# Kernel tuning notes

Hardware: AMD Instinct MI355X
Metric: run time of the kernel (lower is better)

The kernel has to match this reference:

```python
import jax, jax.numpy as jnp
import numpy as np

B, N, D = 8, 1024, 768
H, Z = 12, 64          # num_heads, head_dim (D = H*Z)
HID = 3072             # int(D * mlp_ratio)


def setup_inputs() -> dict:
    key = jax.random.key(0)
    k1, k2, k3, k4 = jax.random.split(key, 4)
    s = 0.02
    x = jax.random.normal(k1, (B, N, D), dtype=jnp.float32)
    Wq = jax.random.normal(k2, (D, D), dtype=jnp.float32) * s
    Wk = jax.random.normal(k3, (D, D), dtype=jnp.float32) * s
    betas = jnp.full((H,), Z ** -0.5, dtype=jnp.float32)
    W_mlp = jax.random.normal(k4, (HID, D), dtype=jnp.float32) * s
    return {"x": x, "Wq": Wq, "Wk": Wk, "betas": betas, "W_mlp": W_mlp}


def reference(x, Wq, Wk, betas, W_mlp):
    # --- KQ-aligned attention ---
    # torch Linear: y = x @ W.T ; weight shape [out=D, in=D]
    Q = jnp.einsum('bnd,ed->bne', x, Wq).reshape(B, N, H, Z).transpose(0, 2, 1, 3)  # bhqz
    K = jnp.einsum('bnd,ed->bne', x, Wk).reshape(B, N, H, Z).transpose(0, 2, 1, 3)  # bhkz
    Wq_r = Wq.reshape(H, Z, D)
    Wk_r = Wk.reshape(H, Z, D)
    F1 = jnp.einsum('hzd,bhkz->bkhd', Wq_r, K)
    F2 = jnp.einsum('hzd,bhqz->bqhd', Wk_r, Q)
    scores = jnp.einsum('bhqz,bhkz,h->bhqk', Q, K, betas)
    attn = jax.nn.softmax(scores, axis=-1)
    T1 = jnp.einsum('bkhd,bhqk->bqd', F1, attn)
    T2 = jnp.einsum('bqhd,bhqk->bkd', F2, attn)
    # --- symmetric-weight Hopfield MLP (bias=False) ---
    hid = jax.nn.relu(jnp.einsum('bnd,hd->bnh', x, W_mlp))
    mlp = jnp.einsum('bnh,hd->bnd', hid, W_mlp)
    return T1 + T2 + mlp
```

## Files before the change

kernel.cpp:

```cpp
#include <hip/hip_runtime.h>
#include <hip/hip_bf16.h>

#define Bq 8
#define Nq 1024
#define Dq 768
#define Hq 12
#define Zq 64
#define HIDq 3072
#define BN (Bq*Nq)
#define QKP 1536

typedef unsigned short u16;
typedef short s16x8 __attribute__((ext_vector_type(8)));
typedef float f32x4 __attribute__((ext_vector_type(4)));
typedef unsigned short u16x4 __attribute__((ext_vector_type(4)));

#define MFMA16 __builtin_amdgcn_mfma_f32_16x16x32_bf16
#define GLOAD16(g, l) __builtin_amdgcn_global_load_lds( \
    (const __attribute__((address_space(1))) void*)(const void*)(g), \
    (__attribute__((address_space(3))) void*)(l), 16, 0, 0)

__device__ __forceinline__ u16 f2bf(float f) {
  unsigned u = __float_as_uint(f);
  return (u16)((u + 0x7FFFu + ((u >> 16) & 1u)) >> 16);
}

__device__ __forceinline__ void xcd_swizzle(int gx, int gy, int& bx, int& by) {
  int l = blockIdx.y * gx + blockIdx.x;
  int c = l & 7, j = l >> 3;
  by = c * (gy >> 3) + j / gx;
  bx = j % gx;
}

__global__ __launch_bounds__(256) void cvt_bf16(const float* __restrict__ in,
                                                u16* __restrict__ out, int n) {
  int i = (blockIdx.x * 256 + threadIdx.x) * 4;
  if (i >= n) return;
  float4 v = *(const float4*)&in[i];
  u16x4 o; o[0] = f2bf(v.x); o[1] = f2bf(v.y); o[2] = f2bf(v.z); o[3] = f2bf(v.w);
  *(u16x4*)&out[i] = o;
}

__global__ __launch_bounds__(256) void cvt_tr(const float* __restrict__ in,
                                              u16* __restrict__ out, u16* __restrict__ outT,
                                              int C, int out_p, int outT_p) {
  __shared__ u16 T[64][72];
  const int t = threadIdx.x;
  const int r0 = blockIdx.y * 64, c0 = blockIdx.x * 64;
  const int r = t >> 3, c8 = (t & 7) * 8;
#pragma unroll
  for (int p = 0; p < 2; p++) {
    const float* ip = &in[(size_t)(r0 + r + p * 32) * C + c0 + c8];
    float4 v0 = *(const float4*)ip, v1 = *(const float4*)(ip + 4);
    u16 tmp[8] = {f2bf(v0.x), f2bf(v0.y), f2bf(v0.z), f2bf(v0.w),
                  f2bf(v1.x), f2bf(v1.y), f2bf(v1.z), f2bf(v1.w)};
    *(uint4*)&out[(size_t)(r0 + r + p * 32) * out_p + c0 + c8] = *(uint4*)tmp;
    *(uint4*)&T[r + p * 32][c8] = *(uint4*)tmp;
  }
  __syncthreads();
#pragma unroll
  for (int p = 0; p < 2; p++) {
    int oc = r + p * 32;
    u16 tmp[8];
#pragma unroll
    for (int j = 0; j < 8; j++) tmp[j] = T[c8 + j][oc];
    *(uint4*)&outT[(size_t)(c0 + oc) * outT_p + r0 + c8] = *(uint4*)tmp;
  }
}

__global__ __launch_bounds__(256) void transpose_bf16(
    const u16* __restrict__ in, u16* __restrict__ out,
    int in_pitch, int out_pitch, int inner_n,
    long in_bs_o, long in_bs_i, long out_bs_o, long out_bs_i) {
  __shared__ u16 T[64][72];
  const int t = threadIdx.x;
  const int bz = blockIdx.z;
  const long iboff = (long)(bz / inner_n) * in_bs_o + (long)(bz % inner_n) * in_bs_i;
  const long oboff = (long)(bz / inner_n) * out_bs_o + (long)(bz % inner_n) * out_bs_i;
  const u16* ip = in + iboff + (long)(blockIdx.y * 64) * in_pitch + blockIdx.x * 64;
  u16* op = out + oboff + (long)(blockIdx.x * 64) * out_pitch + blockIdx.y * 64;
  const int r = t >> 3, c8 = (t & 7) * 8;
#pragma unroll
  for (int p = 0; p < 2; p++)
    *(uint4*)&T[r + p * 32][c8] = *(const uint4*)(ip + (size_t)(r + p * 32) * in_pitch + c8);
  __syncthreads();
#pragma unroll
  for (int p = 0; p < 2; p++) {
    int oc = r + p * 32;
    u16 tmp[8];
#pragma unroll
    for (int j = 0; j < 8; j++) tmp[j] = T[c8 + j][oc];
    *(uint4*)(op + (size_t)oc * out_pitch + c8) = *(uint4*)tmp;
  }
}

template<bool RELU>
__global__ __launch_bounds__(256) void gemm_bf16(
    const u16* __restrict__ A, const u16* __restrict__ B, u16* __restrict__ C,
    int M, int N, int K) {
  __shared__ u16 As[2][128 * 32];
  __shared__ u16 Bs[2][128 * 32];
  int bx, by;
  xcd_swizzle(gridDim.x, gridDim.y, bx, by);
  const int t = threadIdx.x, l = t & 63, w = t >> 6;
  const int lq = l & 15, quad = l >> 4;
  const int bm = by * 128, bn = bx * 128;
  const int wm = (w & 1) * 64, wn = (w >> 1) * 64;
  f32x4 acc[4][4];
#pragma unroll
  for (int i = 0; i < 4; i++)
#pragma unroll
    for (int j = 0; j < 4; j++) acc[i][j] = (f32x4){0.f, 0.f, 0.f, 0.f};

  auto stage = [&](int k0, int bufi) {
#pragma unroll
    for (int p = 0; p < 2; p++) {
      int idx = p * 256 + t;
      GLOAD16(A + (size_t)(bm + (idx >> 2)) * K + k0 + (idx & 3) * 8, &As[bufi][idx * 8]);
      GLOAD16(B + (size_t)(bn + (idx >> 2)) * K + k0 + (idx & 3) * 8, &Bs[bufi][idx * 8]);
    }
  };
  stage(0, 0);
  const int nIter = K >> 5;
  for (int it = 0; it < nIter; it++) {
    __syncthreads();
    if (it + 1 < nIter) stage((it + 1) * 32, (it + 1) & 1);
    const int bi = it & 1;
    s16x8 af[4], bf[4];
#pragma unroll
    for (int mt = 0; mt < 4; mt++)
      af[mt] = *(const s16x8*)&As[bi][(wm + mt * 16 + lq) * 32 + quad * 8];
#pragma unroll
    for (int nt = 0; nt < 4; nt++)
      bf[nt] = *(const s16x8*)&Bs[bi][(wn + nt * 16 + lq) * 32 + quad * 8];
#pragma unroll
    for (int mt = 0; mt < 4; mt++)
#pragma unroll
      for (int nt = 0; nt < 4; nt++)
        acc[mt][nt] = MFMA16(af[mt], bf[nt], acc[mt][nt], 0, 0, 0);
  }
#pragma unroll
  for (int mt = 0; mt < 4; mt++)
#pragma unroll
    for (int nt = 0; nt < 4; nt++) {
      int row = bm + wm + mt * 16 + quad * 4;
      int col = bn + wn + nt * 16 + lq;
#pragma unroll
      for (int r = 0; r < 4; r++) {
        float v = acc[mt][nt][r];
        if (RELU) v = fmaxf(v, 0.f);
        C[(size_t)(row + r) * N + col] = f2bf(v);
      }
    }
}

__global__ __launch_bounds__(256) void gemm_out2(
    const u16* __restrict__ AV12, const u16* __restrict__ hid,
    const u16* __restrict__ WqkT, const u16* __restrict__ WmT,
    float* __restrict__ out) {
  __shared__ u16 As[2][128 * 64];
  __shared__ u16 Bs[2][64 * 64];
  int bx, by;
  xcd_swizzle(gridDim.x, gridDim.y, bx, by);
  const int t = threadIdx.x, l = t & 63, w = t >> 6;
  const int lq = l & 15, quad = l >> 4;
  const int bm = by * 128, bn = bx * 64;
  const int wm = w * 32;
  f32x4 acc[2][4];
#pragma unroll
  for (int i = 0; i < 2; i++)
#pragma unroll
    for (int j = 0; j < 4; j++) acc[i][j] = (f32x4){0.f, 0.f, 0.f, 0.f};

  auto stage = [&](int tl, int bufi) {
    const u16* A; const u16* B; int pitch, k0;
    if (tl < 24) { A = AV12; B = WqkT; pitch = QKP;  k0 = tl * 64; }
    else         { A = hid;  B = WmT;  pitch = HIDq; k0 = (tl - 24) * 64; }
#pragma unroll
    for (int p = 0; p < 4; p++) {
      int idx = p * 256 + t, ks = idx >> 9, rem = idx & 511;
      GLOAD16(A + (size_t)(bm + (rem >> 2)) * pitch + k0 + ks * 32 + (rem & 3) * 8,
              &As[bufi][idx * 8]);
    }
#pragma unroll
    for (int p = 0; p < 2; p++) {
      int idx = p * 256 + t, ks = idx >> 8, rem = idx & 255;
      GLOAD16(B + (size_t)(bn + (rem >> 2)) * pitch + k0 + ks * 32 + (rem & 3) * 8,
              &Bs[bufi][idx * 8]);
    }
  };
  stage(0, 0);
  for (int tl = 0; tl < 72; tl++) {
    __syncthreads();
    if (tl + 1 < 72) stage(tl + 1, (tl + 1) & 1);
    const int bi = tl & 1;
#pragma unroll
    for (int ks = 0; ks < 2; ks++) {
      s16x8 af[2], bf[4];
#pragma unroll
      for (int mt = 0; mt < 2; mt++)
        af[mt] = *(const s16x8*)&As[bi][ks * 4096 + (wm + mt * 16 + lq) * 32 + quad * 8];
#pragma unroll
      for (int nt = 0; nt < 4; nt++)
        bf[nt] = *(const s16x8*)&Bs[bi][ks * 2048 + (nt * 16 + lq) * 32 + quad * 8];
#pragma unroll
      for (int mt = 0; mt < 2; mt++)
#pragma unroll
        for (int nt = 0; nt < 4; nt++)
          acc[mt][nt] = MFMA16(af[mt], bf[nt], acc[mt][nt], 0, 0, 0);
    }
  }
#pragma unroll
  for (int mt = 0; mt < 2; mt++)
#pragma unroll
    for (int nt = 0; nt < 4; nt++) {
      int row = bm + wm + mt * 16 + quad * 4;
      int col = bn + nt * 16 + lq;
#pragma unroll
      for (int r = 0; r < 4; r++)
        out[(size_t)(row + r) * Dq + col] = acc[mt][nt][r];
    }
}

__global__ __launch_bounds__(256) void attn_pass1(
    const u16* __restrict__ QKb, const u16* __restrict__ KbT,
    const float* __restrict__ betas, u16* __restrict__ AV12,
    float* __restrict__ lg) {
  __shared__ u16 Qs[2][64][32];
  __shared__ u16 Ks[2][2][64][32];
  __shared__ u16 Kts[2][2][64][32];
  __shared__ u16 Ps[64][72];
  __shared__ float red[4][64];
  __shared__ float li[64];

  const int t = threadIdx.x, l = t & 63, w = t >> 6;
  const int lq = l & 15, quad = l >> 4;
  const int c = blockIdx.x & 7, j = blockIdx.x >> 3;
  const int bh = c * 12 + j / 16, qt = j % 16;
  const int b = bh / Hq, h = bh % Hq;
  const int q0 = qt * 64;
  const float beta = betas[h];
  const u16* Qh = QKb + (size_t)(b * Nq) * QKP + h * 64;
  const u16* Kh = Qh + Dq;
  const u16* KTh = KbT + (size_t)bh * 64 * Nq;
  u16* QsF = &Qs[0][0][0];

#pragma unroll
  for (int p = 0; p < 2; p++) {
    int idx = p * 256 + t;
    GLOAD16(Qh + (size_t)(q0 + ((idx >> 2) & 63)) * QKP + (idx >> 8) * 32 + (idx & 3) * 8,
            QsF + idx * 8);
  }

  auto stageK = [&](int kt, int bufi) {
#pragma unroll
    for (int p = 0; p < 2; p++) {
      int idx = p * 256 + t;
      GLOAD16(Kh + (size_t)(kt * 64 + ((idx >> 2) & 63)) * QKP + (idx >> 8) * 32 + (idx & 3) * 8,
              &Ks[bufi][0][0][0] + idx * 8);
      GLOAD16(KTh + (size_t)((idx >> 2) & 63) * Nq + kt * 64 + (idx >> 8) * 32 + (idx & 3) * 8,
              &Kts[bufi][0][0][0] + idx * 8);
    }
  };
  stageK(0, 0);
  __syncthreads();
  s16x8 bqf[2][4];
#pragma unroll
  for (int zs = 0; zs < 2; zs++)
#pragma unroll
    for (int nt = 0; nt < 4; nt++)
      bqf[zs][nt] = *(const s16x8*)&Qs[zs][nt * 16 + lq][quad * 8];

  float lsum[4] = {0.f, 0.f, 0.f, 0.f};
  f32x4 ao[4];
#pragma unroll
  for (int nt = 0; nt < 4; nt++) ao[nt] = (f32x4){0.f, 0.f, 0.f, 0.f};

  for (int kt = 0; kt < 16; kt++) {
    if (kt) __syncthreads();
    if (kt + 1 < 16) stageK(kt + 1, (kt + 1) & 1);
    const int bi = kt & 1;
    f32x4 sc[4];
#pragma unroll
    for (int nt = 0; nt < 4; nt++) sc[nt] = (f32x4){0.f, 0.f, 0.f, 0.f};
#pragma unroll
    for (int zs = 0; zs < 2; zs++) {
      s16x8 a = *(const s16x8*)&Ks[bi][zs][w * 16 + lq][quad * 8];
#pragma unroll
      for (int nt = 0; nt < 4; nt++)
        sc[nt] = MFMA16(a, bqf[zs][nt], sc[nt], 0, 0, 0);
    }
#pragma unroll
    for (int nt = 0; nt < 4; nt++) {
      u16x4 pk;
#pragma unroll
      for (int r = 0; r < 4; r++) {
        float e = __expf(sc[nt][r] * beta);
        lsum[nt] += e;
        pk[r] = f2bf(e);
      }
      *(u16x4*)&Ps[nt * 16 + lq][w * 16 + quad * 4] = pk;
    }
    __syncthreads();
#pragma unroll
    for (int ks = 0; ks < 2; ks++) {
      s16x8 a = *(const s16x8*)&Ps[w * 16 + lq][ks * 32 + quad * 8];
#pragma unroll
      for (int nt = 0; nt < 4; nt++) {
        s16x8 bk = *(const s16x8*)&Kts[bi][ks][nt * 16 + lq][quad * 8];
        ao[nt] = MFMA16(a, bk, ao[nt], 0, 0, 0);
      }
    }
  }
#pragma unroll
  for (int nt = 0; nt < 4; nt++) {
    float v = lsum[nt];
    v += __shfl_xor(v, 16, 64);
    v += __shfl_xor(v, 32, 64);
    if (l < 16) red[w][nt * 16 + lq] = v;
  }
  __syncthreads();
  if (t < 64) {
    float s = red[0][t] + red[1][t] + red[2][t] + red[3][t];
    lg[(size_t)bh * Nq + q0 + t] = s;
    li[t] = 1.0f / s;
  }
  __syncthreads();
  u16* Oh = AV12 + (size_t)(b * Nq + q0) * QKP + h * 64;
  float lr[4];
#pragma unroll
  for (int r = 0; r < 4; r++) lr[r] = li[w * 16 + quad * 4 + r];
#pragma unroll
  for (int nt = 0; nt < 4; nt++)
#pragma unroll
    for (int r = 0; r < 4; r++)
      Oh[(size_t)(w * 16 + quad * 4 + r) * QKP + nt * 16 + lq] = f2bf(ao[nt][r] * lr[r]);
}

__global__ __launch_bounds__(256) void attn_pass2(
    const u16* __restrict__ QKb, const u16* __restrict__ QbT,
    const float* __restrict__ betas, u16* __restrict__ AV12,
    const float* __restrict__ lg) {
  __shared__ u16 Ks[2][64][32];
  __shared__ u16 Qs[2][2][64][32];
  __shared__ u16 Qts[2][2][64][32];
  __shared__ u16 Pts[64][72];
  __shared__ float li_s[2][64];

  const int t = threadIdx.x, l = t & 63, w = t >> 6;
  const int lq = l & 15, quad = l >> 4;
  const int c = blockIdx.x & 7, j = blockIdx.x >> 3;
  const int bh = c * 12 + j / 16, kt = j % 16;
  const int b = bh / Hq, h = bh % Hq;
  const int k0 = kt * 64;
  const float beta = betas[h];
  const u16* Qh = QKb + (size_t)(b * Nq) * QKP + h * 64;
  const u16* Kh = Qh + Dq;
  const u16* QTh = QbT + (size_t)bh * 64 * Nq;
  u16* KsF = &Ks[0][0][0];

#pragma unroll
  for (int p = 0; p < 2; p++) {
    int idx = p * 256 + t;
    GLOAD16(Kh + (size_t)(k0 + ((idx >> 2) & 63)) * QKP + (idx >> 8) * 32 + (idx & 3) * 8,
            KsF + idx * 8);
  }

  auto stageQ = [&](int qt, int bufi) {
#pragma unroll
    for (int p = 0; p < 2; p++) {
      int idx = p * 256 + t;
      GLOAD16(Qh + (size_t)(qt * 64 + ((idx >> 2) & 63)) * QKP + (idx >> 8) * 32 + (idx & 3) * 8,
              &Qs[bufi][0][0][0] + idx * 8);
      GLOAD16(QTh + (size_t)((idx >> 2) & 63) * Nq + qt * 64 + (idx >> 8) * 32 + (idx & 3) * 8,
              &Qts[bufi][0][0][0] + idx * 8);
    }
    if (t < 64) li_s[bufi][t] = 1.0f / lg[(size_t)bh * Nq + qt * 64 + t];
  };
  stageQ(0, 0);
  __syncthreads();
  s16x8 bkf[2][4];
#pragma unroll
  for (int zs = 0; zs < 2; zs++)
#pragma unroll
    for (int nt = 0; nt < 4; nt++)
      bkf[zs][nt] = *(const s16x8*)&Ks[zs][nt * 16 + lq][quad * 8];

  f32x4 ao[4];
#pragma unroll
  for (int nt = 0; nt < 4; nt++) ao[nt] = (f32x4){0.f, 0.f, 0.f, 0.f};

  for (int qt = 0; qt < 16; qt++) {
    if (qt) __syncthreads();
    if (qt + 1 < 16) stageQ(qt + 1, (qt + 1) & 1);
    const int bi = qt & 1;
    f32x4 sc[4];
#pragma unroll
    for (int nt = 0; nt < 4; nt++) sc[nt] = (f32x4){0.f, 0.f, 0.f, 0.f};
#pragma unroll
    for (int zs = 0; zs < 2; zs++) {
      s16x8 a = *(const s16x8*)&Qs[bi][zs][w * 16 + lq][quad * 8];
#pragma unroll
      for (int nt = 0; nt < 4; nt++)
        sc[nt] = MFMA16(a, bkf[zs][nt], sc[nt], 0, 0, 0);
    }
    float lr[4];
#pragma unroll
    for (int r = 0; r < 4; r++) lr[r] = li_s[bi][w * 16 + quad * 4 + r];
#pragma unroll
    for (int nt = 0; nt < 4; nt++) {
      u16x4 pk;
#pragma unroll
      for (int r = 0; r < 4; r++)
        pk[r] = f2bf(__expf(sc[nt][r] * beta) * lr[r]);
      *(u16x4*)&Pts[nt * 16 + lq][w * 16 + quad * 4] = pk;
    }
    __syncthreads();
#pragma unroll
    for (int qs = 0; qs < 2; qs++) {
      s16x8 a = *(const s16x8*)&Pts[w * 16 + lq][qs * 32 + quad * 8];
#pragma unroll
      for (int nt = 0; nt < 4; nt++) {
        s16x8 bq = *(const s16x8*)&Qts[bi][qs][nt * 16 + lq][quad * 8];
        ao[nt] = MFMA16(a, bq, ao[nt], 0, 0, 0);
      }
    }
  }
  u16* Oh = AV12 + (size_t)(b * Nq + k0) * QKP + Dq + h * 64;
#pragma unroll
  for (int nt = 0; nt < 4; nt++)
#pragma unroll
    for (int r = 0; r < 4; r++)
      Oh[(size_t)(w * 16 + quad * 4 + r) * QKP + nt * 16 + lq] = f2bf(ao[nt][r]);
}

extern "C" void kernel_launch(void* const* d_in, const int* in_sizes, int n_in,
                              void* d_out, int out_size, void* d_ws, size_t ws_size,
                              hipStream_t stream) {
  const float* x     = (const float*)d_in[0];
  const float* Wq    = (const float*)d_in[1];
  const float* Wk    = (const float*)d_in[2];
  const float* betas = (const float*)d_in[3];
  const float* Wm    = (const float*)d_in[4];
  float* out = (float*)d_out;

  u16* xb   = (u16*)d_ws;
  u16* Wqkb = xb + (size_t)BN * Dq;
  u16* Wmb  = Wqkb + (size_t)QKP * Dq;
  u16* WqkT = Wmb + (size_t)HIDq * Dq;
  u16* QKb  = WqkT + (size_t)Dq * QKP;
  u16* QbT  = QKb + (size_t)BN * QKP;
  u16* KbT  = QbT + (size_t)Bq * Hq * Zq * Nq;
  u16* AV12 = KbT + (size_t)Bq * Hq * Zq * Nq;
  float* lg = (float*)(AV12 + (size_t)BN * QKP);
  u16* hidb = QKb;
  u16* WmT  = xb;

  dim3 blk(256);
  cvt_bf16<<<(BN * Dq) / 1024, blk, 0, stream>>>(x, xb, BN * Dq);
  cvt_tr<<<dim3(12, 12), blk, 0, stream>>>(Wq, Wqkb, WqkT, Dq, Dq, QKP);
  cvt_tr<<<dim3(12, 12), blk, 0, stream>>>(Wk, Wqkb + (size_t)Dq * Dq, WqkT + Dq, Dq, Dq, QKP);
  cvt_bf16<<<(HIDq * Dq) / 1024, blk, 0, stream>>>(Wm, Wmb, HIDq * Dq);

  gemm_bf16<false><<<dim3(QKP / 128, BN / 128), blk, 0, stream>>>(
      xb, Wqkb, QKb, BN, QKP, Dq);

  transpose_bf16<<<dim3(1, 16, 96), blk, 0, stream>>>(QKb, QbT, QKP, Nq, Hq,
      (long)Nq * QKP, 64, (long)Hq * 64 * Nq, (long)64 * Nq);
  transpose_bf16<<<dim3(1, 16, 96), blk, 0, stream>>>(QKb + Dq, KbT, QKP, Nq, Hq,
      (long)Nq * QKP, 64, (long)Hq * 64 * Nq, (long)64 * Nq);

  attn_pass1<<<Bq * Hq * 16, blk, 0, stream>>>(QKb, KbT, betas, AV12, lg);
  attn_pass2<<<Bq * Hq * 16, blk, 0, stream>>>(QKb, QbT, betas, AV12, lg);

  gemm_bf16<true><<<dim3(HIDq / 128, BN / 128), blk, 0, stream>>>(
      xb, Wmb, hidb, BN, HIDq, Dq);

  transpose_bf16<<<dim3(12, 48, 1), blk, 0, stream>>>(Wmb, WmT, Dq, HIDq, 1, 0, 0, 0, 0);

  gemm_out2<<<dim3(Dq / 64, BN / 128), blk, 0, stream>>>(AV12, hidb, WqkT, WmT, out);
}
```

Before: 372.4 us.

## Cut attention LDS footprint by single-buffering score operands and aliasing scratch buffers

```diff
diff --git a/kernel.cpp b/kernel.cpp
--- a/kernel.cpp
+++ b/kernel.cpp
@@ -23,6 +23,13 @@
 __device__ __forceinline__ u16 f2bf(float f) {
   unsigned u = __float_as_uint(f);
   return (u16)((u + 0x7FFFu + ((u >> 16) & 1u)) >> 16);
+}
+
+__device__ __forceinline__ unsigned pk2bf(float a, float b) {
+  union { __hip_bfloat162 h; unsigned u; } cv;
+  cv.h.x = __float2bfloat16(a);
+  cv.h.y = __float2bfloat16(b);
+  return cv.u;
 }
 
 __device__ __forceinline__ void xcd_swizzle(int gx, int gy, int& bx, int& by) {
@@ -226,12 +233,9 @@
     const u16* __restrict__ QKb, const u16* __restrict__ KbT,
     const float* __restrict__ betas, u16* __restrict__ AV12,
     float* __restrict__ lg) {
-  __shared__ u16 Qs[2][64][32];
-  __shared__ u16 Ks[2][2][64][32];
+  __shared__ u16 Ps[64][72];
+  __shared__ u16 Ks[2][64][32];
   __shared__ u16 Kts[2][2][64][32];
-  __shared__ u16 Ps[64][72];
-  __shared__ float red[4][64];
-  __shared__ float li[64];
 
   const int t = threadIdx.x, l = t & 63, w = t >> 6;
   const int lq = l & 15, quad = l >> 4;
@@ -243,7 +247,25 @@
   const u16* Qh = QKb + (size_t)(b * Nq) * QKP + h * 64;
   const u16* Kh = Qh + Dq;
   const u16* KTh = KbT + (size_t)bh * 64 * Nq;
-  u16* QsF = &Qs[0][0][0];
+  u16* QsF = &Ps[0][0];
+  u16* KsF = &Ks[0][0][0];
+
+  auto stageK = [&](int kt2) {
+#pragma unroll
+    for (int p = 0; p < 2; p++) {
+      int idx = p * 256 + t;
+      GLOAD16(Kh + (size_t)(kt2 * 64 + ((idx >> 2) & 63)) * QKP + (idx >> 8) * 32 + (idx & 3) * 8,
+              KsF + idx * 8);
+    }
+  };
+  auto stageKt = [&](int kt2, int bufi) {
+#pragma unroll
+    for (int p = 0; p < 2; p++) {
+      int idx = p * 256 + t;
+      GLOAD16(KTh + (size_t)((idx >> 2) & 63) * Nq + kt2 * 64 + (idx >> 8) * 32 + (idx & 3) * 8,
+              &Kts[bufi][0][0][0] + idx * 8);
+    }
+  };
 
 #pragma unroll
   for (int p = 0; p < 2; p++) {
@@ -251,25 +273,16 @@
     GLOAD16(Qh + (size_t)(q0 + ((idx >> 2) & 63)) * QKP + (idx >> 8) * 32 + (idx & 3) * 8,
             QsF + idx * 8);
   }
-
-  auto stageK = [&](int kt, int bufi) {
-#pragma unroll
-    for (int p = 0; p < 2; p++) {
-      int idx = p * 256 + t;
-      GLOAD16(Kh + (size_t)(kt * 64 + ((idx >> 2) & 63)) * QKP + (idx >> 8) * 32 + (idx & 3) * 8,
-              &Ks[bufi][0][0][0] + idx * 8);
-      GLOAD16(KTh + (size_t)((idx >> 2) & 63) * Nq + kt * 64 + (idx >> 8) * 32 + (idx & 3) * 8,
-              &Kts[bufi][0][0][0] + idx * 8);
-    }
-  };
-  stageK(0, 0);
+  stageK(0);
+  stageKt(0, 0);
   __syncthreads();
   s16x8 bqf[2][4];
 #pragma unroll
   for (int zs = 0; zs < 2; zs++)
 #pragma unroll
     for (int nt = 0; nt < 4; nt++)
-      bqf[zs][nt] = *(const s16x8*)&Qs[zs][nt * 16 + lq][quad * 8];
+      bqf[zs][nt] = *(const s16x8*)&QsF[zs * 2048 + (nt * 16 + lq) * 32 + quad * 8];
+  __syncthreads();
 
   float lsum[4] = {0.f, 0.f, 0.f, 0.f};
   f32x4 ao[4];
@@ -278,30 +291,30 @@
 
   for (int kt = 0; kt < 16; kt++) {
     if (kt) __syncthreads();
-    if (kt + 1 < 16) stageK(kt + 1, (kt + 1) & 1);
     const int bi = kt & 1;
     f32x4 sc[4];
 #pragma unroll
     for (int nt = 0; nt < 4; nt++) sc[nt] = (f32x4){0.f, 0.f, 0.f, 0.f};
 #pragma unroll
     for (int zs = 0; zs < 2; zs++) {
-      s16x8 a = *(const s16x8*)&Ks[bi][zs][w * 16 + lq][quad * 8];
+      s16x8 a = *(const s16x8*)&Ks[zs][w * 16 + lq][quad * 8];
 #pragma unroll
       for (int nt = 0; nt < 4; nt++)
         sc[nt] = MFMA16(a, bqf[zs][nt], sc[nt], 0, 0, 0);
     }
 #pragma unroll
     for (int nt = 0; nt < 4; nt++) {
-      u16x4 pk;
-#pragma unroll
-      for (int r = 0; r < 4; r++) {
-        float e = __expf(sc[nt][r] * beta);
-        lsum[nt] += e;
-        pk[r] = f2bf(e);
-      }
-      *(u16x4*)&Ps[nt * 16 + lq][w * 16 + quad * 4] = pk;
+      float e0 = __expf(sc[nt][0] * beta), e1 = __expf(sc[nt][1] * beta);
+      float e2 = __expf(sc[nt][2] * beta), e3 = __expf(sc[nt][3] * beta);
+      lsum[nt] += (e0 + e1) + (e2 + e3);
+      uint2 pk; pk.x = pk2bf(e0, e1); pk.y = pk2bf(e2, e3);
+      *(uint2*)&Ps[nt * 16 + lq][w * 16 + quad * 4] = pk;
     }
     __syncthreads();
+    if (kt + 1 < 16) {
+      stageK(kt + 1);
+      stageKt(kt + 1, (kt + 1) & 1);
+    }
 #pragma unroll
     for (int ks = 0; ks < 2; ks++) {
       s16x8 a = *(const s16x8*)&Ps[w * 16 + lq][ks * 32 + quad * 8];
@@ -312,24 +325,27 @@
       }
     }
   }
+  __syncthreads();
+  float* redp = (float*)&Kts[0][0][0][0];
+  float* lip  = redp + 256;
 #pragma unroll
   for (int nt = 0; nt < 4; nt++) {
     float v = lsum[nt];
     v += __shfl_xor(v, 16, 64);
     v += __shfl_xor(v, 32, 64);
-    if (l < 16) red[w][nt * 16 + lq] = v;
+    if (l < 16) redp[w * 64 + nt * 16 + lq] = v;
   }
   __syncthreads();
   if (t < 64) {
-    float s = red[0][t] + red[1][t] + red[2][t] + red[3][t];
+    float s = redp[t] + redp[64 + t] + redp[128 + t] + redp[192 + t];
     lg[(size_t)bh * Nq + q0 + t] = s;
-    li[t] = 1.0f / s;
+    lip[t] = 1.0f / s;
   }
   __syncthreads();
   u16* Oh = AV12 + (size_t)(b * Nq + q0) * QKP + h * 64;
   float lr[4];
 #pragma unroll
-  for (int r = 0; r < 4; r++) lr[r] = li[w * 16 + quad * 4 + r];
+  for (int r = 0; r < 4; r++) lr[r] = lip[w * 16 + quad * 4 + r];
 #pragma unroll
   for (int nt = 0; nt < 4; nt++)
 #pragma unroll
@@ -341,10 +357,9 @@
     const u16* __restrict__ QKb, const u16* __restrict__ QbT,
     const float* __restrict__ betas, u16* __restrict__ AV12,
     const float* __restrict__ lg) {
-  __shared__ u16 Ks[2][64][32];
-  __shared__ u16 Qs[2][2][64][32];
+  __shared__ u16 Pts[64][72];
+  __shared__ u16 Qs[2][64][32];
   __shared__ u16 Qts[2][2][64][32];
-  __shared__ u16 Pts[64][72];
   __shared__ float li_s[2][64];
 
   const int t = threadIdx.x, l = t & 63, w = t >> 6;
@@ -357,7 +372,25 @@
   const u16* Qh = QKb + (size_t)(b * Nq) * QKP + h * 64;
   const u16* Kh = Qh + Dq;
   const u16* QTh = QbT + (size_t)bh * 64 * Nq;
-  u16* KsF = &Ks[0][0][0];
+  u16* KsF = &Pts[0][0];
+  u16* QsF = &Qs[0][0][0];
+
+  auto stageQ = [&](int qt2) {
+#pragma unroll
+    for (int p = 0; p < 2; p++) {
+      int idx = p * 256 + t;
+      GLOAD16(Qh + (size_t)(qt2 * 64 + ((idx >> 2) & 63)) * QKP + (idx >> 8) * 32 + (idx & 3) * 8,
+              QsF + idx * 8);
+    }
+  };
+  auto stageQt = [&](int qt2, int bufi) {
+#pragma unroll
+    for (int p = 0; p < 2; p++) {
+      int idx = p * 256 + t;
+      GLOAD16(QTh + (size_t)((idx >> 2) & 63) * Nq + qt2 * 64 + (idx >> 8) * 32 + (idx & 3) * 8,
+              &Qts[bufi][0][0][0] + idx * 8);
+    }
+  };
 
 #pragma unroll
   for (int p = 0; p < 2; p++) {
@@ -365,26 +398,17 @@
     GLOAD16(Kh + (size_t)(k0 + ((idx >> 2) & 63)) * QKP + (idx >> 8) * 32 + (idx & 3) * 8,
             KsF + idx * 8);
   }
-
-  auto stageQ = [&](int qt, int bufi) {
-#pragma unroll
-    for (int p = 0; p < 2; p++) {
-      int idx = p * 256 + t;
-      GLOAD16(Qh + (size_t)(qt * 64 + ((idx >> 2) & 63)) * QKP + (idx >> 8) * 32 + (idx & 3) * 8,
-              &Qs[bufi][0][0][0] + idx * 8);
-      GLOAD16(QTh + (size_t)((idx >> 2) & 63) * Nq + qt * 64 + (idx >> 8) * 32 + (idx & 3) * 8,
-              &Qts[bufi][0][0][0] + idx * 8);
-    }
-    if (t < 64) li_s[bufi][t] = 1.0f / lg[(size_t)bh * Nq + qt * 64 + t];
-  };
-  stageQ(0, 0);
+  stageQ(0);
+  stageQt(0, 0);
+  if (t < 64) li_s[0][t] = 1.0f / lg[(size_t)bh * Nq + t];
   __syncthreads();
   s16x8 bkf[2][4];
 #pragma unroll
   for (int zs = 0; zs < 2; zs++)
 #pragma unroll
     for (int nt = 0; nt < 4; nt++)
-      bkf[zs][nt] = *(const s16x8*)&Ks[zs][nt * 16 + lq][quad * 8];
+      bkf[zs][nt] = *(const s16x8*)&KsF[zs * 2048 + (nt * 16 + lq) * 32 + quad * 8];
+  __syncthreads();
 
   f32x4 ao[4];
 #pragma unroll
@@ -392,14 +416,13 @@
 
   for (int qt = 0; qt < 16; qt++) {
     if (qt) __syncthreads();
-    if (qt + 1 < 16) stageQ(qt + 1, (qt + 1) & 1);
     const int bi = qt & 1;
     f32x4 sc[4];
 #pragma unroll
     for (int nt = 0; nt < 4; nt++) sc[nt] = (f32x4){0.f, 0.f, 0.f, 0.f};
 #pragma unroll
     for (int zs = 0; zs < 2; zs++) {
-      s16x8 a = *(const s16x8*)&Qs[bi][zs][w * 16 + lq][quad * 8];
+      s16x8 a = *(const s16x8*)&Qs[zs][w * 16 + lq][quad * 8];
 #pragma unroll
       for (int nt = 0; nt < 4; nt++)
         sc[nt] = MFMA16(a, bkf[zs][nt], sc[nt], 0, 0, 0);
@@ -409,13 +432,19 @@
     for (int r = 0; r < 4; r++) lr[r] = li_s[bi][w * 16 + quad * 4 + r];
 #pragma unroll
     for (int nt = 0; nt < 4; nt++) {
-      u16x4 pk;
-#pragma unroll
-      for (int r = 0; r < 4; r++)
-        pk[r] = f2bf(__expf(sc[nt][r] * beta) * lr[r]);
-      *(u16x4*)&Pts[nt * 16 + lq][w * 16 + quad * 4] = pk;
+      float e0 = __expf(sc[nt][0] * beta) * lr[0];
+      float e1 = __expf(sc[nt][1] * beta) * lr[1];
+      float e2 = __expf(sc[nt][2] * beta) * lr[2];
+      float e3 = __expf(sc[nt][3] * beta) * lr[3];
+      uint2 pk; pk.x = pk2bf(e0, e1); pk.y = pk2bf(e2, e3);
+      *(uint2*)&Pts[nt * 16 + lq][w * 16 + quad * 4] = pk;
     }
     __syncthreads();
+    if (qt + 1 < 16) {
+      stageQ(qt + 1);
+      stageQt(qt + 1, (qt + 1) & 1);
+      if (t < 64) li_s[(qt + 1) & 1][t] = 1.0f / lg[(size_t)bh * Nq + (qt + 1) * 64 + t];
+    }
 #pragma unroll
     for (int qs = 0; qs < 2; qs++) {
       s16x8 a = *(const s16x8*)&Pts[w * 16 + lq][qs * 32 + quad * 8];
```

After: 359.5 us. 3.5% less time.

## Keep attention probabilities in registers via shuffles and merge conversion/transpose launches

Applied to the files above, without the earlier changes.

```diff
diff --git a/kernel.cpp b/kernel.cpp
--- a/kernel.cpp
+++ b/kernel.cpp
@@ -25,6 +25,13 @@
   return (u16)((u + 0x7FFFu + ((u >> 16) & 1u)) >> 16);
 }
 
+__device__ __forceinline__ unsigned pk2bf(float a, float b) {
+  union { __hip_bfloat162 h; unsigned u; } cv;
+  cv.h.x = __float2bfloat16(a);
+  cv.h.y = __float2bfloat16(b);
+  return cv.u;
+}
+
 __device__ __forceinline__ void xcd_swizzle(int gx, int gy, int& bx, int& by) {
   int l = blockIdx.y * gx + blockIdx.x;
   int c = l & 7, j = l >> 3;
@@ -32,29 +39,36 @@
   bx = j % gx;
 }
 
-__global__ __launch_bounds__(256) void cvt_bf16(const float* __restrict__ in,
-                                                u16* __restrict__ out, int n) {
-  int i = (blockIdx.x * 256 + threadIdx.x) * 4;
-  if (i >= n) return;
+__global__ __launch_bounds__(256) void cvt2(const float* __restrict__ x, u16* __restrict__ xb,
+                                            const float* __restrict__ Wm, u16* __restrict__ Wmb) {
+  int bid = blockIdx.x;
+  const float* in; u16* out; int i;
+  if (bid < 6144) { in = x;  out = xb;  i = bid * 1024 + threadIdx.x * 4; }
+  else            { in = Wm; out = Wmb; i = (bid - 6144) * 1024 + threadIdx.x * 4; }
   float4 v = *(const float4*)&in[i];
   u16x4 o; o[0] = f2bf(v.x); o[1] = f2bf(v.y); o[2] = f2bf(v.z); o[3] = f2bf(v.w);
   *(u16x4*)&out[i] = o;
 }
 
-__global__ __launch_bounds__(256) void cvt_tr(const float* __restrict__ in,
-                                              u16* __restrict__ out, u16* __restrict__ outT,
-                                              int C, int out_p, int outT_p) {
+__global__ __launch_bounds__(256) void cvt_tr2(const float* __restrict__ Wq,
+                                               const float* __restrict__ Wk,
+                                               u16* __restrict__ Wqkb,
+                                               u16* __restrict__ WqkT) {
   __shared__ u16 T[64][72];
   const int t = threadIdx.x;
+  const int z = blockIdx.z;
+  const float* in = z ? Wk : Wq;
+  u16* out = Wqkb + (size_t)z * Dq * Dq;
+  u16* outT = WqkT + z * Dq;
   const int r0 = blockIdx.y * 64, c0 = blockIdx.x * 64;
   const int r = t >> 3, c8 = (t & 7) * 8;
 #pragma unroll
   for (int p = 0; p < 2; p++) {
-    const float* ip = &in[(size_t)(r0 + r + p * 32) * C + c0 + c8];
+    const float* ip = &in[(size_t)(r0 + r + p * 32) * Dq + c0 + c8];
     float4 v0 = *(const float4*)ip, v1 = *(const float4*)(ip + 4);
     u16 tmp[8] = {f2bf(v0.x), f2bf(v0.y), f2bf(v0.z), f2bf(v0.w),
                   f2bf(v1.x), f2bf(v1.y), f2bf(v1.z), f2bf(v1.w)};
-    *(uint4*)&out[(size_t)(r0 + r + p * 32) * out_p + c0 + c8] = *(uint4*)tmp;
+    *(uint4*)&out[(size_t)(r0 + r + p * 32) * Dq + c0 + c8] = *(uint4*)tmp;
     *(uint4*)&T[r + p * 32][c8] = *(uint4*)tmp;
   }
   __syncthreads();
@@ -64,7 +78,7 @@
     u16 tmp[8];
 #pragma unroll
     for (int j = 0; j < 8; j++) tmp[j] = T[c8 + j][oc];
-    *(uint4*)&outT[(size_t)(c0 + oc) * outT_p + r0 + c8] = *(uint4*)tmp;
+    *(uint4*)&outT[(size_t)(c0 + oc) * QKP + r0 + c8] = *(uint4*)tmp;
   }
 }
 
@@ -91,6 +105,32 @@
 #pragma unroll
     for (int j = 0; j < 8; j++) tmp[j] = T[c8 + j][oc];
     *(uint4*)(op + (size_t)oc * out_pitch + c8) = *(uint4*)tmp;
+  }
+}
+
+__global__ __launch_bounds__(256) void head_tr(const u16* __restrict__ QKb,
+                                               u16* __restrict__ QbT,
+                                               u16* __restrict__ KbT) {
+  __shared__ u16 T[64][72];
+  const int t = threadIdx.x;
+  const int z = blockIdx.z;
+  const int half = (z >= 96) ? 1 : 0;
+  const int bhh = z - 96 * half;
+  const u16* ip = QKb + (size_t)(bhh / Hq) * Nq * QKP + (bhh % Hq) * 64 + half * Dq
+                + (size_t)(blockIdx.y * 64) * QKP;
+  u16* op = (half ? KbT : QbT) + (size_t)bhh * 64 * Nq + blockIdx.y * 64;
+  const int r = t >> 3, c8 = (t & 7) * 8;
+#pragma unroll
+  for (int p = 0; p < 2; p++)
+    *(uint4*)&T[r + p * 32][c8] = *(const uint4*)(ip + (size_t)(r + p * 32) * QKP + c8);
+  __syncthreads();
+#pragma unroll
+  for (int p = 0; p < 2; p++) {
+    int oc = r + p * 32;
+    u16 tmp[8];
+#pragma unroll
+    for (int j = 0; j < 8; j++) tmp[j] = T[c8 + j][oc];
+    *(uint4*)(op + (size_t)oc * Nq + c8) = *(uint4*)tmp;
   }
 }
 
@@ -229,9 +269,6 @@
   __shared__ u16 Qs[2][64][32];
   __shared__ u16 Ks[2][2][64][32];
   __shared__ u16 Kts[2][2][64][32];
-  __shared__ u16 Ps[64][72];
-  __shared__ float red[4][64];
-  __shared__ float li[64];
 
   const int t = threadIdx.x, l = t & 63, w = t >> 6;
   const int lq = l & 15, quad = l >> 4;
@@ -243,14 +280,6 @@
   const u16* Qh = QKb + (size_t)(b * Nq) * QKP + h * 64;
   const u16* Kh = Qh + Dq;
   const u16* KTh = KbT + (size_t)bh * 64 * Nq;
-  u16* QsF = &Qs[0][0][0];
-
-#pragma unroll
-  for (int p = 0; p < 2; p++) {
-    int idx = p * 256 + t;
-    GLOAD16(Qh + (size_t)(q0 + ((idx >> 2) & 63)) * QKP + (idx >> 8) * 32 + (idx & 3) * 8,
-            QsF + idx * 8);
-  }
 
   auto stageK = [&](int kt, int bufi) {
 #pragma unroll
@@ -262,74 +291,77 @@
               &Kts[bufi][0][0][0] + idx * 8);
     }
   };
+#pragma unroll
+  for (int p = 0; p < 2; p++) {
+    int idx = p * 256 + t;
+    GLOAD16(Qh + (size_t)(q0 + ((idx >> 2) & 63)) * QKP + (idx >> 8) * 32 + (idx & 3) * 8,
+            &Qs[0][0][0] + idx * 8);
+  }
   stageK(0, 0);
   __syncthreads();
-  s16x8 bqf[2][4];
+  s16x8 bqf[2];
 #pragma unroll
   for (int zs = 0; zs < 2; zs++)
-#pragma unroll
-    for (int nt = 0; nt < 4; nt++)
-      bqf[zs][nt] = *(const s16x8*)&Qs[zs][nt * 16 + lq][quad * 8];
-
-  float lsum[4] = {0.f, 0.f, 0.f, 0.f};
+    bqf[zs] = *(const s16x8*)&Qs[zs][w * 16 + lq][quad * 8];
+
+  float lsum = 0.f;
   f32x4 ao[4];
 #pragma unroll
   for (int nt = 0; nt < 4; nt++) ao[nt] = (f32x4){0.f, 0.f, 0.f, 0.f};
 
+  const int ybase = lq + ((quad & 1) << 5);
   for (int kt = 0; kt < 16; kt++) {
     if (kt) __syncthreads();
     if (kt + 1 < 16) stageK(kt + 1, (kt + 1) & 1);
     const int bi = kt & 1;
     f32x4 sc[4];
 #pragma unroll
-    for (int nt = 0; nt < 4; nt++) sc[nt] = (f32x4){0.f, 0.f, 0.f, 0.f};
-#pragma unroll
-    for (int zs = 0; zs < 2; zs++) {
-      s16x8 a = *(const s16x8*)&Ks[bi][zs][w * 16 + lq][quad * 8];
-#pragma unroll
-      for (int nt = 0; nt < 4; nt++)
-        sc[nt] = MFMA16(a, bqf[zs][nt], sc[nt], 0, 0, 0);
-    }
-#pragma unroll
-    for (int nt = 0; nt < 4; nt++) {
-      u16x4 pk;
-#pragma unroll
-      for (int r = 0; r < 4; r++) {
-        float e = __expf(sc[nt][r] * beta);
-        lsum[nt] += e;
-        pk[r] = f2bf(e);
-      }
-      *(u16x4*)&Ps[nt * 16 + lq][w * 16 + quad * 4] = pk;
-    }
-    __syncthreads();
-#pragma unroll
-    for (int ks = 0; ks < 2; ks++) {
-      s16x8 a = *(const s16x8*)&Ps[w * 16 + lq][ks * 32 + quad * 8];
+    for (int s = 0; s < 4; s++) sc[s] = (f32x4){0.f, 0.f, 0.f, 0.f};
+#pragma unroll
+    for (int zs = 0; zs < 2; zs++)
+#pragma unroll
+      for (int s = 0; s < 4; s++) {
+        s16x8 a = *(const s16x8*)&Ks[bi][zs][s * 16 + lq][quad * 8];
+        sc[s] = MFMA16(a, bqf[zs], sc[s], 0, 0, 0);
+      }
+    unsigned pw[4][2];
+#pragma unroll
+    for (int s = 0; s < 4; s++) {
+      float e0 = __expf(sc[s][0] * beta), e1 = __expf(sc[s][1] * beta);
+      float e2 = __expf(sc[s][2] * beta), e3 = __expf(sc[s][3] * beta);
+      lsum += (e0 + e1) + (e2 + e3);
+      pw[s][0] = pk2bf(e0, e1);
+      pw[s][1] = pk2bf(e2, e3);
+    }
+#pragma unroll
+    for (int m = 0; m < 2; m++) {
+      union { unsigned u[4]; s16x8 v; } af;
+#pragma unroll
+      for (int p = 0; p < 4; p++) {
+        int y = ybase + ((p >> 1) << 4);
+        unsigned lo = (unsigned)__shfl((int)pw[2 * m][p & 1], y, 64);
+        unsigned hi = (unsigned)__shfl((int)pw[2 * m + 1][p & 1], y, 64);
+        af.u[p] = (quad < 2) ? lo : hi;
+      }
 #pragma unroll
       for (int nt = 0; nt < 4; nt++) {
-        s16x8 bk = *(const s16x8*)&Kts[bi][ks][nt * 16 + lq][quad * 8];
-        ao[nt] = MFMA16(a, bk, ao[nt], 0, 0, 0);
-      }
-    }
-  }
-#pragma unroll
-  for (int nt = 0; nt < 4; nt++) {
-    float v = lsum[nt];
-    v += __shfl_xor(v, 16, 64);
-    v += __shfl_xor(v, 32, 64);
-    if (l < 16) red[w][nt * 16 + lq] = v;
-  }
-  __syncthreads();
-  if (t < 64) {
-    float s = red[0][t] + red[1][t] + red[2][t] + red[3][t];
-    lg[(size_t)bh * Nq + q0 + t] = s;
-    li[t] = 1.0f / s;
-  }
-  __syncthreads();
+        s16x8 bk = *(const s16x8*)&Kts[bi][m][nt * 16 + lq][quad * 8];
+        ao[nt] = MFMA16(af.v, bk, ao[nt], 0, 0, 0);
+      }
+    }
+  }
+  float v = lsum;
+  v += __shfl_xor(v, 16, 64);
+  v += __shfl_xor(v, 32, 64);
+  float* lip = (float*)&Qs[0][0][0];
+  if (l < 16) {
+    lg[(size_t)bh * Nq + q0 + w * 16 + lq] = v;
+    lip[w * 16 + lq] = 1.0f / v;
+  }
+  float lr[4];
+#pragma unroll
+  for (int r = 0; r < 4; r++) lr[r] = lip[w * 16 + quad * 4 + r];
   u16* Oh = AV12 + (size_t)(b * Nq + q0) * QKP + h * 64;
-  float lr[4];
-#pragma unroll
-  for (int r = 0; r < 4; r++) lr[r] = li[w * 16 + quad * 4 + r];
 #pragma unroll
   for (int nt = 0; nt < 4; nt++)
 #pragma unroll
@@ -341,11 +373,9 @@
     const u16* __restrict__ QKb, const u16* __restrict__ QbT,
     const float* __restrict__ betas, u16* __restrict__ AV12,
     const float* __restrict__ lg) {
-  __shared__ u16 Ks[2][64][32];
   __shared__ u16 Qs[2][2][64][32];
   __shared__ u16 Qts[2][2][64][32];
-  __shared__ u16 Pts[64][72];
-  __shared__ float li_s[2][64];
+  __shared__ u16 KsS[2][64][32];
 
   const int t = threadIdx.x, l = t & 63, w = t >> 6;
   const int lq = l & 15, quad = l >> 4;
@@ -357,72 +387,82 @@
   const u16* Qh = QKb + (size_t)(b * Nq) * QKP + h * 64;
   const u16* Kh = Qh + Dq;
   const u16* QTh = QbT + (size_t)bh * 64 * Nq;
-  u16* KsF = &Ks[0][0][0];
-
+  float* lis = (float*)&KsS[0][0][0];
+
+  auto stageQ = [&](int qt2, int bufi) {
+#pragma unroll
+    for (int p = 0; p < 2; p++) {
+      int idx = p * 256 + t;
+      GLOAD16(Qh + (size_t)(qt2 * 64 + ((idx >> 2) & 63)) * QKP + (idx >> 8) * 32 + (idx & 3) * 8,
+              &Qs[bufi][0][0][0] + idx * 8);
+      GLOAD16(QTh + (size_t)((idx >> 2) & 63) * Nq + qt2 * 64 + (idx >> 8) * 32 + (idx & 3) * 8,
+              &Qts[bufi][0][0][0] + idx * 8);
+    }
+  };
 #pragma unroll
   for (int p = 0; p < 2; p++) {
     int idx = p * 256 + t;
     GLOAD16(Kh + (size_t)(k0 + ((idx >> 2) & 63)) * QKP + (idx >> 8) * 32 + (idx & 3) * 8,
-            KsF + idx * 8);
-  }
-
-  auto stageQ = [&](int qt, int bufi) {
-#pragma unroll
-    for (int p = 0; p < 2; p++) {
-      int idx = p * 256 + t;
-      GLOAD16(Qh + (size_t)(qt * 64 + ((idx >> 2) & 63)) * QKP + (idx >> 8) * 32 + (idx & 3) * 8,
-              &Qs[bufi][0][0][0] + idx * 8);
-      GLOAD16(QTh + (size_t)((idx >> 2) & 63) * Nq + qt * 64 + (idx >> 8) * 32 + (idx & 3) * 8,
-              &Qts[bufi][0][0][0] + idx * 8);
-    }
-    if (t < 64) li_s[bufi][t] = 1.0f / lg[(size_t)bh * Nq + qt * 64 + t];
-  };
+            &KsS[0][0][0] + idx * 8);
+  }
   stageQ(0, 0);
   __syncthreads();
-  s16x8 bkf[2][4];
+  s16x8 bkw[2];
 #pragma unroll
   for (int zs = 0; zs < 2; zs++)
-#pragma unroll
-    for (int nt = 0; nt < 4; nt++)
-      bkf[zs][nt] = *(const s16x8*)&Ks[zs][nt * 16 + lq][quad * 8];
+    bkw[zs] = *(const s16x8*)&KsS[zs][w * 16 + lq][quad * 8];
+  __syncthreads();
+  if (t < 64) lis[t] = 1.0f / lg[(size_t)bh * Nq + t];
+  __syncthreads();
 
   f32x4 ao[4];
 #pragma unroll
   for (int nt = 0; nt < 4; nt++) ao[nt] = (f32x4){0.f, 0.f, 0.f, 0.f};
 
-  for (int qt = 0; qt < 16; qt++) {
-    if (qt) __syncthreads();
-    if (qt + 1 < 16) stageQ(qt + 1, (qt + 1) & 1);
-    const int bi = qt & 1;
+  const int ybase = lq + ((quad & 1) << 5);
+  for (int qt2 = 0; qt2 < 16; qt2++) {
+    if (qt2) __syncthreads();
+    if (qt2 + 1 < 16) {
+      stageQ(qt2 + 1, (qt2 + 1) & 1);
+      if (t < 64)
+        lis[((qt2 + 1) & 1) * 64 + t] = 1.0f / lg[(size_t)bh * Nq + (qt2 + 1) * 64 + t];
+    }
+    const int bi = qt2 & 1;
     f32x4 sc[4];
 #pragma unroll
-    for (int nt = 0; nt < 4; nt++) sc[nt] = (f32x4){0.f, 0.f, 0.f, 0.f};
-#pragma unroll
-    for (int zs = 0; zs < 2; zs++) {
-      s16x8 a = *(const s16x8*)&Qs[bi][zs][w * 16 + lq][quad * 8];
-#pragma unroll
-      for (int nt = 0; nt < 4; nt++)
-        sc[nt] = MFMA16(a, bkf[zs][nt], sc[nt], 0, 0, 0);
-    }
-    float lr[4];
-#pragma unroll
-    for (int r = 0; r < 4; r++) lr[r] = li_s[bi][w * 16 + quad * 4 + r];
-#pragma unroll
-    for (int nt = 0; nt < 4; nt++) {
-      u16x4 pk;
-#pragma unroll
-      for (int r = 0; r < 4; r++)
-        pk[r] = f2bf(__expf(sc[nt][r] * beta) * lr[r]);
-      *(u16x4*)&Pts[nt * 16 + lq][w * 16 + quad * 4] = pk;
-    }
-    __syncthreads();
-#pragma unroll
-    for (int qs = 0; qs < 2; qs++) {
-      s16x8 a = *(const s16x8*)&Pts[w * 16 + lq][qs * 32 + quad * 8];
+    for (int s = 0; s < 4; s++) sc[s] = (f32x4){0.f, 0.f, 0.f, 0.f};
+#pragma unroll
+    for (int zs = 0; zs < 2; zs++)
+#pragma unroll
+      for (int s = 0; s < 4; s++) {
+        s16x8 a = *(const s16x8*)&Qs[bi][zs][s * 16 + lq][quad * 8];
+        sc[s] = MFMA16(a, bkw[zs], sc[s], 0, 0, 0);
+      }
+    unsigned pw[4][2];
+#pragma unroll
+    for (int s = 0; s < 4; s++) {
+      int qi = bi * 64 + s * 16 + quad * 4;
+      float e0 = __expf(sc[s][0] * beta) * lis[qi + 0];
+      float e1 = __expf(sc[s][1] * beta) * lis[qi + 1];
+      float e2 = __expf(sc[s][2] * beta) * lis[qi + 2];
+      float e3 = __expf(sc[s][3] * beta) * lis[qi + 3];
+      pw[s][0] = pk2bf(e0, e1);
+      pw[s][1] = pk2bf(e2, e3);
+    }
+#pragma unroll
+    for (int m = 0; m < 2; m++) {
+      union { unsigned u[4]; s16x8 v; } af;
+#pragma unroll
+      for (int p = 0; p < 4; p++) {
+        int y = ybase + ((p >> 1) << 4);
+        unsigned lo = (unsigned)__shfl((int)pw[2 * m][p & 1], y, 64);
+        unsigned hi = (unsigned)__shfl((int)pw[2 * m + 1][p & 1], y, 64);
+        af.u[p] = (quad < 2) ? lo : hi;
+      }
 #pragma unroll
       for (int nt = 0; nt < 4; nt++) {
-        s16x8 bq = *(const s16x8*)&Qts[bi][qs][nt * 16 + lq][quad * 8];
-        ao[nt] = MFMA16(a, bq, ao[nt], 0, 0, 0);
+        s16x8 bq = *(const s16x8*)&Qts[bi][m][nt * 16 + lq][quad * 8];
+        ao[nt] = MFMA16(af.v, bq, ao[nt], 0, 0, 0);
       }
     }
   }
@@ -457,18 +497,13 @@
   u16* WmT  = xb;
 
   dim3 blk(256);
-  cvt_bf16<<<(BN * Dq) / 1024, blk, 0, stream>>>(x, xb, BN * Dq);
-  cvt_tr<<<dim3(12, 12), blk, 0, stream>>>(Wq, Wqkb, WqkT, Dq, Dq, QKP);
-  cvt_tr<<<dim3(12, 12), blk, 0, stream>>>(Wk, Wqkb + (size_t)Dq * Dq, WqkT + Dq, Dq, Dq, QKP);
-  cvt_bf16<<<(HIDq * Dq) / 1024, blk, 0, stream>>>(Wm, Wmb, HIDq * Dq);
+  cvt2<<<8448, blk, 0, stream>>>(x, xb, Wm, Wmb);
+  cvt_tr2<<<dim3(12, 12, 2), blk, 0, stream>>>(Wq, Wk, Wqkb, WqkT);
 
   gemm_bf16<false><<<dim3(QKP / 128, BN / 128), blk, 0, stream>>>(
       xb, Wqkb, QKb, BN, QKP, Dq);
 
-  transpose_bf16<<<dim3(1, 16, 96), blk, 0, stream>>>(QKb, QbT, QKP, Nq, Hq,
-      (long)Nq * QKP, 64, (long)Hq * 64 * Nq, (long)64 * Nq);
-  transpose_bf16<<<dim3(1, 16, 96), blk, 0, stream>>>(QKb + Dq, KbT, QKP, Nq, Hq,
-      (long)Nq * QKP, 64, (long)Hq * 64 * Nq, (long)64 * Nq);
+  head_tr<<<dim3(1, 16, 192), blk, 0, stream>>>(QKb, QbT, KbT);
 
   attn_pass1<<<Bq * Hq * 16, blk, 0, stream>>>(QKb, KbT, betas, AV12, lg);
   attn_pass2<<<Bq * Hq * 16, blk, 0, stream>>>(QKb, QbT, betas, AV12, lg);
```

New measurement: 379.2 us. No clear change (+1.8%).
